# Kernel optimization log

Hardware: AMD Instinct MI355X
Metric: run time of the kernel (lower is better)

The kernel has to match this reference:

```python
import jax, jax.numpy as jnp
import numpy as np

K_ATTRS = 16  # fixed number of attribute clusters (torch.unique made static for jit)
NEG_INF = jnp.float32(-1e9)


def setup_inputs() -> dict:
    key = jax.random.key(0)
    ks = jax.random.split(key, 20)
    B, T, V, D, H = 4096, 200, 100000, 64, 64
    M0, M1 = 256, 128
    FC_IN = D + D + H + D  # 256
    s = 0.02
    f32 = jnp.float32
    inp = {
        "item_id": jax.random.randint(ks[0], (B,), 0, V),
        "hist_item_ids": jax.random.randint(ks[1], (B, T), 0, V),
        "hist_item_attributes": jax.random.randint(ks[2], (B, T), 0, K_ATTRS),
        "emb_table": s * jax.random.normal(ks[3], (V, D), dtype=f32),
        "au_W1": s * jax.random.normal(ks[4], (4 * D, H), dtype=f32),
        "au_b1": jnp.zeros((H,), f32),
        "au_W2": s * jax.random.normal(ks[5], (H, 1), dtype=f32),
        "au_b2": jnp.zeros((1,), f32),
        "gru_Wx": s * jax.random.normal(ks[6], (D, 3 * H), dtype=f32),
        "gru_Wh": s * jax.random.normal(ks[7], (H, 3 * H), dtype=f32),
        "gru_b": jnp.zeros((3 * H,), f32),
        "fc_W0": s * jax.random.normal(ks[8], (FC_IN, M0), dtype=f32),
        "fc_b0": jnp.zeros((M0,), f32),
        "fc_W1": s * jax.random.normal(ks[9], (M0, M1), dtype=f32),
        "fc_b1": jnp.zeros((M1,), f32),
        "final_W": s * jax.random.normal(ks[10], (M1, 1), dtype=f32),
        "final_b": jnp.zeros((1,), f32),
    }
    return inp


def reference(item_id, hist_item_ids, hist_item_attributes, emb_table,
              au_W1, au_b1, au_W2, au_b2, gru_Wx, gru_Wh, gru_b,
              fc_W0, fc_b0, fc_W1, fc_b1, final_W, final_b):
    item = emb_table[item_id]            # [B,D]
    hist = emb_table[hist_item_ids]      # [B,T,D]
    B = item.shape[0]
    H = gru_Wh.shape[0]

    # --- DIEN: GRU over history, final hidden state ---
    xp = hist @ gru_Wx + gru_b           # [B,T,3H]

    def step(h, x):
        gz, gr, gn = jnp.split(h @ gru_Wh, 3, axis=-1)
        xz, xr, xn = jnp.split(x, 3, axis=-1)
        z = jax.nn.sigmoid(xz + gz)
        r = jax.nn.sigmoid(xr + gr)
        n = jnp.tanh(xn + r * gn)
        return (1.0 - z) * n + z * h, None

    h0 = jnp.zeros((B, H), hist.dtype)
    interest_evolution, _ = jax.lax.scan(step, h0, jnp.swapaxes(xp, 0, 1))  # [B,H]

    # --- DIN-style activation unit: score each key against the target item ---
    def act_unit(q, keys):  # q:[B,D], keys:[B,N,D] -> [B,N,1]
        qe = jnp.broadcast_to(q[:, None, :], keys.shape)
        feat = jnp.concatenate([keys, qe, keys - qe, keys * qe], axis=-1)
        hid = jax.nn.relu(feat @ au_W1 + au_b1)
        return hid @ au_W2 + au_b2

    w1 = act_unit(item, hist)                    # [B,T,1]
    user_interest_l1 = jnp.sum(w1 * hist, axis=1)  # [B,D]

    # --- attribute_group: per-attribute masked softmax + weighted sum ---
    mask = hist_item_attributes[..., None] == jnp.arange(K_ATTRS)  # [B,T,K]
    logits = jnp.where(mask, w1, NEG_INF)        # [B,T,K]
    probs = jax.nn.softmax(logits, axis=1) * mask
    cluster = jnp.einsum('btk,btd->bkd', probs, hist)  # [B,K,D]

    w2 = act_unit(item, cluster)                 # [B,K,1]
    user_interest_l2 = jnp.sum(w2 * cluster, axis=1)  # [B,D]

    combined = jnp.concatenate(
        [user_interest_l1, user_interest_l2, interest_evolution, item], axis=1)
    x = jax.nn.relu(combined @ fc_W0 + fc_b0)
    x = jax.nn.relu(x @ fc_W1 + fc_b1)
    out = x @ final_W + final_b                  # [B,1]
    return jax.nn.sigmoid(out[:, 0])             # [B]
```

## Files before the change

### kernel.cpp

```cpp
#include <hip/hip_runtime.h>
#include <hip/hip_bf16.h>

#define B_   4096
#define T_   200
#define KA   16

#define OFF_BG  0
#define OFF_WQ  4096
#define OFF_QP  (OFF_BG  + B_*T_)
#define OFF_UI1 (OFF_QP  + B_*64)
#define OFF_UI2 (OFF_UI1 + B_*64)
#define OFF_HF  (OFF_UI2 + B_*64)
#define OFF_CL  (OFF_HF  + B_*64)

typedef __attribute__((ext_vector_type(8))) short bf16x8;
typedef __attribute__((ext_vector_type(4))) float f32x4;

__device__ __forceinline__ float sigmoidf_(float x) {
  return 1.f / (1.f + __expf(-x));
}
__device__ __forceinline__ float sigf(float x) {
  return __builtin_amdgcn_rcpf(1.f + __builtin_amdgcn_exp2f(-1.44269504f * x));
}
__device__ __forceinline__ float tanhfast(float y) {
  return 1.f - 2.f * __builtin_amdgcn_rcpf(1.f + __builtin_amdgcn_exp2f(2.88539008f * y));
}
__device__ __forceinline__ short f2bf(float x) {
  unsigned u = __float_as_uint(x);
  unsigned r = (u + 0x7fffu + ((u >> 16) & 1u)) >> 16;
  return (short)r;
}
__device__ __forceinline__ unsigned cvtpk(float lo, float hi) {
  unsigned r;
  asm("v_cvt_pk_bf16_f32 %0, %1, %2" : "=v"(r) : "v"(lo), "v"(hi));
  return r;
}
union BF8 { bf16x8 v; unsigned u[4]; };

__device__ __forceinline__ bf16x8 pack8(float4 f0, float4 f1) {
  BF8 a;
  a.u[0] = cvtpk(f0.x, f0.y);
  a.u[1] = cvtpk(f0.z, f0.w);
  a.u[2] = cvtpk(f1.x, f1.y);
  a.u[3] = cvtpk(f1.z, f1.w);
  return a.v;
}
__device__ __forceinline__ bf16x8 pack8m(float4 f0, float4 f1,
                                         float4 q0, float4 q1) {
  BF8 a;
  a.u[0] = cvtpk(f0.x*q0.x, f0.y*q0.y);
  a.u[1] = cvtpk(f0.z*q0.z, f0.w*q0.w);
  a.u[2] = cvtpk(f1.x*q1.x, f1.y*q1.y);
  a.u[3] = cvtpk(f1.z*q1.z, f1.w*q1.w);
  return a.v;
}


__global__ __launch_bounds__(256) void k_prep(
    const float* __restrict__ auW1, short* __restrict__ bg,
    float* __restrict__ wq)
{
  const int i = blockIdx.x*256 + threadIdx.x;
  if (i < 8192) {
    const int k = i >> 6, col = i & 63;
    float v;
    if (k < 64) v = auW1[k*64 + col] + auW1[2*4096 + k*64 + col];
    else        v = auW1[3*4096 + (k-64)*64 + col];
    bg[((k >> 5)*4 + ((k >> 3) & 3))*512 + col*8 + (k & 7)] = f2bf(v);
  } else if (i < 12288) {
    const int j = i - 8192;
    wq[j] = auW1[(64 + (j >> 6))*64 + (j & 63)]
          - auW1[(128 + (j >> 6))*64 + (j & 63)];
  }
}

__global__ __launch_bounds__(256) void k_act1(
    const int* __restrict__ item_id, const int* __restrict__ hist_ids,
    const int* __restrict__ attrs,
    const float* __restrict__ emb, const float* __restrict__ aub1,
    const float* __restrict__ auW2, const float* __restrict__ aub2,
    const short* __restrict__ bg_in, const float* __restrict__ wq_in,
    float* __restrict__ qp_out, float* __restrict__ ui1_out,
    float* __restrict__ ui2_out)
{
  __shared__ __align__(16) char sPool[16384];
  __shared__ __align__(16) float sCl[16][72];
  __shared__ float sW1[208];
  __shared__ float sP[200];
  __shared__ float sM[KA], sE[KA];
  __shared__ float sItem[64], sQp[64];
  __shared__ float sQpP[4][64];
  __shared__ float sUi[4][64];
  __shared__ float sWf[16];
  __shared__ int   sIds[200], sAttr[200];

  short* sB2 = (short*)sPool;
  float (*sAcc)[KA][64] = (float (*)[KA][64])sPool;

  const int b = blockIdx.x;
  const int tid = threadIdx.x;
  const int wave = tid >> 6, lane = tid & 63;
  const int g = lane >> 4;
  const int c15 = lane & 15;
  const int itrow = item_id[b];

  for (int i = tid; i < 4096; i += 256)
    ((unsigned*)sB2)[i] = ((const unsigned*)bg_in)[i];
  if (tid < 64) sItem[tid] = emb[(size_t)itrow*64 + tid];
  if (tid < T_) {
    sIds[tid]  = hist_ids[(size_t)b*T_ + tid];
    sAttr[tid] = attrs[(size_t)b*T_ + tid];
  }
  __syncthreads();

  {
    const int j = tid & 63, iq = tid >> 6;
    float acc = 0.f;
    #pragma unroll
    for (int ii = 0; ii < 16; ++ii) {
      const int i = iq*16 + ii;
      acc += sItem[i] * wq_in[i*64 + j];
    }
    sQpP[iq][j] = acc;
  }
  __syncthreads();
  if (tid < 64) {
    float q = aub1[tid] + sQpP[0][tid] + sQpP[1][tid] + sQpP[2][tid] + sQpP[3][tid];
    sQp[tid] = q;
    qp_out[(size_t)b*64 + tid] = q;
  }
  __syncthreads();

  const float4* itemp = (const float4*)(emb + (size_t)itrow*64);
  float4 q0 = itemp[g*2],     q1 = itemp[g*2 + 1];
  float4 q2 = itemp[8 + g*2], q3 = itemp[8 + g*2 + 1];

  bf16x8 bfr[4][4];
  #pragma unroll
  for (int kk = 0; kk < 4; ++kk) {
    #pragma unroll
    for (int n = 0; n < 4; ++n)
      bfr[kk][n] = *(const bf16x8*)&sB2[(kk*4 + g)*512 + (n*16 + c15)*8];
  }
  float w2v[4], qpv[4];
  #pragma unroll
  for (int n = 0; n < 4; ++n) {
    w2v[n] = auW2[n*16 + c15];
    qpv[n] = sQp[n*16 + c15];
  }
  const float b2v = aub2[0];
  __syncthreads();

  for (int i = tid; i < 4*KA*64; i += 256) ((float*)sAcc)[i] = 0.f;

  {
    float4 c0, c1, c2, c3;
    {
      const int t = wave*16 + c15;
      const int tc = (t < T_) ? t : (T_ - 1);
      const float4* kp = (const float4*)(emb + (size_t)sIds[tc]*64);
      c0 = kp[g*2];     c1 = kp[g*2 + 1];
      c2 = kp[8 + g*2]; c3 = kp[8 + g*2 + 1];
    }
    for (int tt = wave; tt < 13; tt += 4) {
      float4 n0{0,0,0,0}, n1{0,0,0,0}, n2{0,0,0,0}, n3{0,0,0,0};
      const int ttn = tt + 4;
      if (ttn < 13) {
        const int t = ttn*16 + c15;
        const int tc = (t < T_) ? t : (T_ - 1);
        const float4* kp = (const float4*)(emb + (size_t)sIds[tc]*64);
        n0 = kp[g*2];     n1 = kp[g*2 + 1];
        n2 = kp[8 + g*2]; n3 = kp[8 + g*2 + 1];
      }

      bf16x8 a0 = pack8(c0, c1);
      bf16x8 a1 = pack8(c2, c3);
      bf16x8 a2 = pack8m(c0, c1, q0, q1);
      bf16x8 a3 = pack8m(c2, c3, q2, q3);

      f32x4 acc[4];
      #pragma unroll
      for (int n = 0; n < 4; ++n) acc[n] = f32x4{qpv[n], qpv[n], qpv[n], qpv[n]};
      #pragma unroll
      for (int n = 0; n < 4; ++n) {
        acc[n] = __builtin_amdgcn_mfma_f32_16x16x32_bf16(a0, bfr[0][n], acc[n], 0, 0, 0);
        acc[n] = __builtin_amdgcn_mfma_f32_16x16x32_bf16(a1, bfr[1][n], acc[n], 0, 0, 0);
        acc[n] = __builtin_amdgcn_mfma_f32_16x16x32_bf16(a2, bfr[2][n], acc[n], 0, 0, 0);
        acc[n] = __builtin_amdgcn_mfma_f32_16x16x32_bf16(a3, bfr[3][n], acc[n], 0, 0, 0);
      }
      float ws[4] = {0.f, 0.f, 0.f, 0.f};
      #pragma unroll
      for (int n = 0; n < 4; ++n) {
        #pragma unroll
        for (int r = 0; r < 4; ++r)
          ws[r] += fmaxf(acc[n][r], 0.f) * w2v[n];
      }
      #pragma unroll
      for (int r = 0; r < 4; ++r) {
        ws[r] += __shfl_xor(ws[r], 1);
        ws[r] += __shfl_xor(ws[r], 2);
        ws[r] += __shfl_xor(ws[r], 4);
        ws[r] += __shfl_xor(ws[r], 8);
        ws[r] += b2v;
      }
      if (c15 == 0) {
        #pragma unroll
        for (int r = 0; r < 4; ++r) {
          const int trow = tt*16 + g*4 + r;
          if (trow < T_) sW1[trow] = ws[r];
        }
      }
      c0 = n0; c1 = n1; c2 = n2; c3 = n3;
    }
  }
  __syncthreads();

  for (int k = wave; k < KA; k += 4) {
    float m = -1e9f;
    for (int tt4 = 0; tt4 < 4; ++tt4) {
      int t = tt4*64 + lane;
      if (t < T_ && sAttr[t] == k) m = fmaxf(m, sW1[t]);
    }
    #pragma unroll
    for (int off = 32; off > 0; off >>= 1) m = fmaxf(m, __shfl_xor(m, off));
    float e = 0.f;
    for (int tt4 = 0; tt4 < 4; ++tt4) {
      int t = tt4*64 + lane;
      if (t < T_ && sAttr[t] == k) e += __expf(sW1[t] - m);
    }
    #pragma unroll
    for (int off = 32; off > 0; off >>= 1) e += __shfl_xor(e, off);
    if (lane == 0) { sM[k] = m; sE[k] = e; }
  }
  __syncthreads();
  if (tid < T_) {
    int k = sAttr[tid];
    float e = sE[k];
    sP[tid] = (e > 0.f) ? __expf(sW1[tid] - sM[k]) * __builtin_amdgcn_rcpf(e) : 0.f;
  }
  __syncthreads();

  {
    float uiacc = 0.f;
    float vcur = emb[(size_t)sIds[wave]*64 + lane];
    for (int t = wave; t < T_; t += 4) {
      const int tn = t + 4;
      float vnext = 0.f;
      if (tn < T_) vnext = emb[(size_t)sIds[tn]*64 + lane];
      const int k = sAttr[t];
      sAcc[wave][k][lane] += sP[t] * vcur;
      uiacc += sW1[t] * vcur;
      vcur = vnext;
    }
    sUi[wave][lane] = uiacc;
  }
  __syncthreads();

  for (int i = tid; i < KA*64; i += 256) {
    const int k = i >> 6, f = i & 63;
    sCl[k][f] = sAcc[0][0][i] + sAcc[1][0][i] + sAcc[2][0][i] + sAcc[3][0][i];
  }
  if (tid < 64) {
    ui1_out[(size_t)b*64 + tid] =
        sUi[0][tid] + sUi[1][tid] + sUi[2][tid] + sUi[3][tid];
  }
  __syncthreads();

  {
    float4 cl0 = *(const float4*)&sCl[c15][g*8];
    float4 cl1 = *(const float4*)&sCl[c15][g*8 + 4];
    float4 cl2 = *(const float4*)&sCl[c15][32 + g*8];
    float4 cl3 = *(const float4*)&sCl[c15][32 + g*8 + 4];
    bf16x8 a0 = pack8(cl0, cl1);
    bf16x8 a1 = pack8(cl2, cl3);
    bf16x8 a2 = pack8m(cl0, cl1, q0, q1);
    bf16x8 a3 = pack8m(cl2, cl3, q2, q3);

    f32x4 acc[4];
    #pragma unroll
    for (int n = 0; n < 4; ++n) acc[n] = f32x4{qpv[n], qpv[n], qpv[n], qpv[n]};
    #pragma unroll
    for (int n = 0; n < 4; ++n) {
      acc[n] = __builtin_amdgcn_mfma_f32_16x16x32_bf16(a0, bfr[0][n], acc[n], 0, 0, 0);
      acc[n] = __builtin_amdgcn_mfma_f32_16x16x32_bf16(a1, bfr[1][n], acc[n], 0, 0, 0);
      acc[n] = __builtin_amdgcn_mfma_f32_16x16x32_bf16(a2, bfr[2][n], acc[n], 0, 0, 0);
      acc[n] = __builtin_amdgcn_mfma_f32_16x16x32_bf16(a3, bfr[3][n], acc[n], 0, 0, 0);
    }
    float ws[4] = {0.f, 0.f, 0.f, 0.f};
    #pragma unroll
    for (int n = 0; n < 4; ++n) {
      #pragma unroll
      for (int r = 0; r < 4; ++r)
        ws[r] += fmaxf(acc[n][r], 0.f) * w2v[n];
    }
    #pragma unroll
    for (int r = 0; r < 4; ++r) {
      ws[r] += __shfl_xor(ws[r], 1);
      ws[r] += __shfl_xor(ws[r], 2);
      ws[r] += __shfl_xor(ws[r], 4);
      ws[r] += __shfl_xor(ws[r], 8);
    }
    if (wave == 0 && c15 == 0) {
      #pragma unroll
      for (int r = 0; r < 4; ++r) sWf[g*4 + r] = ws[r] + b2v;
    }
  }
  __syncthreads();

  {
    float uiacc = 0.f;
    #pragma unroll
    for (int kk = 0; kk < 4; ++kk) {
      const int k = wave*4 + kk;
      uiacc += sWf[k] * sCl[k][lane];
    }
    sUi[wave][lane] = uiacc;
  }
  __syncthreads();
  if (tid < 64) {
    ui2_out[(size_t)b*64 + tid] =
        sUi[0][tid] + sUi[1][tid] + sUi[2][tid] + sUi[3][tid];
  }
}

#define GRU_ROWS 16
__global__ __launch_bounds__(512) void k_gru(
    const int* __restrict__ hist_ids, const float* __restrict__ emb,
    const float* __restrict__ Wx, const float* __restrict__ Wh,
    const float* __restrict__ gb, float* __restrict__ hfin_out)
{
  __shared__ short sH[2][16*64];
  __shared__ short sX[4][16*64];
  __shared__ int   sIds[16*200];

  const int tid  = threadIdx.x;
  const int w    = tid >> 6;
  const int lane = tid & 63;
  const int g    = lane >> 4;
  const int c15  = lane & 15;
  const int b0   = blockIdx.x * GRU_ROWS;

  for (int i = tid; i < 16*200; i += 512) {
    const int r = i / 200, t = i - r*200;
    sIds[i] = hist_ids[(size_t)(b0 + r)*T_ + t];
  }
  for (int i = tid; i < 16*64; i += 512) sH[0][i] = 0;
  __syncthreads();

  if (w >= 4) {
    const int stane = (w - 4)*64 + lane;
    const int srow  = stane >> 4;
    const int scol  = (stane & 15) * 4;
    const int sidx  = srow*64 + (((scol >> 3) ^ (srow & 7))*8) + (scol & 7);
    const int* idrow = &sIds[srow*200];
    #pragma unroll
    for (int p = 0; p < 2; ++p) {
      const float4 f = *(const float4*)(emb + (size_t)idrow[p]*64 + scol);
      uint2 u; u.x = cvtpk(f.x, f.y); u.y = cvtpk(f.z, f.w);
      *(uint2*)&sX[p][sidx] = u;
    }
    __syncthreads();
    for (int t = 0; t < T_; ++t) {
      const int t2 = (t + 2 < T_) ? (t + 2) : (T_ - 1);
      const float4 f = *(const float4*)(emb + (size_t)idrow[t2]*64 + scol);
      uint2 u; u.x = cvtpk(f.x, f.y); u.y = cvtpk(f.z, f.w);
      *(uint2*)&sX[(t + 2) & 3][sidx] = u;
      __syncthreads();
    }
  } else {
    bf16x8 bx[3][2], bh[3][2];
    #pragma unroll
    for (int l = 0; l < 3; ++l) {
      const int jb = (l*4 + w)*16 + c15;
      #pragma unroll
      for (int kk = 0; kk < 2; ++kk) {
        bf16x8 vx, vh;
        #pragma unroll
        for (int e = 0; e < 8; ++e) {
          const int krow = kk*32 + g*8 + e;
          vx[e] = f2bf(Wx[(size_t)krow*192 + jb]);
          vh[e] = f2bf(Wh[(size_t)krow*192 + jb]);
        }
        bx[l][kk] = vx; bh[l][kk] = vh;
      }
    }
    float bias[3];
    #pragma unroll
    for (int l = 0; l < 3; ++l) bias[l] = gb[l*64 + w*16 + c15];

    const int rs = c15 & 7;
    const int ridx0 = c15*64 + ((g    ) ^ rs)*8;
    const int ridx1 = c15*64 + ((g + 4) ^ rs)*8;
    int widx[4];
    {
      const int unit = w*2 + (c15 >> 3);
      #pragma unroll
      for (int r = 0; r < 4; ++r) {
        const int row = g*4 + r;
        widx[r] = row*64 + ((unit ^ (row & 7))*8) + (c15 & 7);
      }
    }
    float hold[4] = {0.f, 0.f, 0.f, 0.f};
    __syncthreads();

    #pragma unroll 2
    for (int t = 0; t < T_; ++t) {
      const short* hbuf = sH[t & 1];
      short*       hnxt = sH[(t & 1) ^ 1];
      const short* xbuf = sX[t & 3];

      bf16x8 ax0 = *(const bf16x8*)&xbuf[ridx0];
      bf16x8 ax1 = *(const bf16x8*)&xbuf[ridx1];
      bf16x8 ah0 = *(const bf16x8*)&hbuf[ridx0];
      bf16x8 ah1 = *(const bf16x8*)&hbuf[ridx1];

      f32x4 aX[3], aH[3];
      #pragma unroll
      for (int l = 0; l < 3; ++l) {
        aX[l] = f32x4{bias[l], bias[l], bias[l], bias[l]};
        aH[l] = f32x4{0.f, 0.f, 0.f, 0.f};
      }
      #pragma unroll
      for (int l = 0; l < 3; ++l) {
        aH[l] = __builtin_amdgcn_mfma_f32_16x16x32_bf16(ah0, bh[l][0], aH[l], 0, 0, 0);
        aH[l] = __builtin_amdgcn_mfma_f32_16x16x32_bf16(ah1, bh[l][1], aH[l], 0, 0, 0);
        aX[l] = __builtin_amdgcn_mfma_f32_16x16x32_bf16(ax0, bx[l][0], aX[l], 0, 0, 0);
        aX[l] = __builtin_amdgcn_mfma_f32_16x16x32_bf16(ax1, bx[l][1], aX[l], 0, 0, 0);
      }

      #pragma unroll
      for (int r = 0; r < 4; ++r) {
        float z  = sigf(aX[0][r] + aH[0][r]);
        float rr = sigf(aX[1][r] + aH[1][r]);
        float nn = tanhfast(aX[2][r] + rr * aH[2][r]);
        hold[r] = nn + z * (hold[r] - nn);
        hnxt[widx[r]] = f2bf(hold[r]);
      }
      __syncthreads();
    }

    #pragma unroll
    for (int r = 0; r < 4; ++r)
      hfin_out[(size_t)(b0 + g*4 + r)*64 + w*16 + c15] = hold[r];
  }
}

#define MLP_ROWS 16
__global__ __launch_bounds__(256) void k_mlp(
    const int* __restrict__ item_id, const float* __restrict__ emb,
    const float* __restrict__ ui1, const float* __restrict__ ui2,
    const float* __restrict__ hfin,
    const float* __restrict__ W0, const float* __restrict__ b0,
    const float* __restrict__ W1, const float* __restrict__ b1,
    const float* __restrict__ fW, const float* __restrict__ fb,
    float* __restrict__ out)
{
  __shared__ float sC[MLP_ROWS][256];
  __shared__ float sX0[MLP_ROWS][256];
  __shared__ float sX1[MLP_ROWS][128];
  const int tid = threadIdx.x;
  const int rb  = blockIdx.x * MLP_ROWS;

  for (int idx = tid; idx < MLP_ROWS*256; idx += 256) {
    int r = idx >> 8, c = idx & 255;
    size_t row = (size_t)(rb + r);
    float v;
    if (c < 64)       v = ui1[row*64 + c];
    else if (c < 128) v = ui2[row*64 + (c-64)];
    else if (c < 192) v = hfin[row*64 + (c-128)];
    else              v = emb[(size_t)item_id[row]*64 + (c-192)];
    sC[r][c] = v;
  }
  __syncthreads();
  {
    float acc[MLP_ROWS];
    #pragma unroll
    for (int r = 0; r < MLP_ROWS; ++r) acc[r] = b0[tid];
    #pragma unroll 4
    for (int i = 0; i < 256; ++i) {
      float w = W0[(size_t)i*256 + tid];
      #pragma unroll
      for (int r = 0; r < MLP_ROWS; ++r) acc[r] += sC[r][i] * w;
    }
    #pragma unroll
    for (int r = 0; r < MLP_ROWS; ++r) sX0[r][tid] = fmaxf(acc[r], 0.f);
  }
  __syncthreads();
  if (tid < 128) {
    float acc[MLP_ROWS];
    #pragma unroll
    for (int r = 0; r < MLP_ROWS; ++r) acc[r] = b1[tid];
    #pragma unroll 4
    for (int i = 0; i < 256; ++i) {
      float w = W1[(size_t)i*128 + tid];
      #pragma unroll
      for (int r = 0; r < MLP_ROWS; ++r) acc[r] += sX0[r][i] * w;
    }
    #pragma unroll
    for (int r = 0; r < MLP_ROWS; ++r) sX1[r][tid] = fmaxf(acc[r], 0.f);
  }
  __syncthreads();
  {
    int r = tid >> 4, l16 = tid & 15;
    float p = 0.f;
    for (int i = l16; i < 128; i += 16) p += sX1[r][i] * fW[i];
    #pragma unroll
    for (int off = 8; off > 0; off >>= 1) p += __shfl_xor(p, off);
    if (l16 == 0) {
      float logit = p + fb[0];
      out[rb + r] = sigmoidf_(logit);
    }
  }
}

extern "C" void kernel_launch(void* const* d_in, const int* in_sizes, int n_in,
                              void* d_out, int out_size, void* d_ws, size_t ws_size,
                              hipStream_t stream)
{
  const int*   item_id  = (const int*)d_in[0];
  const int*   hist_ids = (const int*)d_in[1];
  const int*   attrs    = (const int*)d_in[2];
  const float* emb      = (const float*)d_in[3];
  const float* auW1     = (const float*)d_in[4];
  const float* aub1     = (const float*)d_in[5];
  const float* auW2     = (const float*)d_in[6];
  const float* aub2     = (const float*)d_in[7];
  const float* gWx      = (const float*)d_in[8];
  const float* gWh      = (const float*)d_in[9];
  const float* gb       = (const float*)d_in[10];
  const float* W0       = (const float*)d_in[11];
  const float* b0       = (const float*)d_in[12];
  const float* W1       = (const float*)d_in[13];
  const float* b1       = (const float*)d_in[14];
  const float* fW       = (const float*)d_in[15];
  const float* fb       = (const float*)d_in[16];

  float* out = (float*)d_out;
  float* ws  = (float*)d_ws;
  short* bg      = (short*)(ws + OFF_BG);
  float* wq      = ws + OFF_WQ;
  float* qp      = ws + OFF_QP;
  float* ui1     = ws + OFF_UI1;
  float* ui2     = ws + OFF_UI2;
  float* hfin    = ws + OFF_HF;

  k_prep<<<48, 256, 0, stream>>>(auW1, bg, wq);
  k_act1<<<B_, 256, 0, stream>>>(item_id, hist_ids, attrs, emb, aub1,
                                 auW2, aub2, bg, wq, qp, ui1, ui2);
  k_gru<<<B_/GRU_ROWS, 512, 0, stream>>>(hist_ids, emb, gWx, gWh, gb, hfin);
  k_mlp<<<B_/MLP_ROWS, 256, 0, stream>>>(item_id, emb, ui1, ui2, hfin,
                                         W0, b0, W1, b1, fW, fb, out);
}
```

Before: 342.1 us.

## Merge GRU and activation-unit kernels into one heterogeneous launch

Combines the GRU recurrence kernel and the per-row attention/cluster kernel into a single launch. The first 256 blocks run the GRU and the remaining 4096 blocks run the attention work, so the latency-bound serial GRU blocks can overlap with the throughput-bound attention blocks. The attention path is widened to 512 threads: more waves share the score tiles, and the weighted-sum and cluster-accumulation loops are split across the two wave halves. The trade-off is a shared 28KB LDS pool and 512-thread blocks for every block, which may reduce occupancy for the attention path. The software prefetch of the next history tile is also removed.

```diff
diff --git a/kernel.cpp b/kernel.cpp
--- a/kernel.cpp
+++ b/kernel.cpp
@@ -11,7 +11,8 @@
 #define OFF_UI1 (OFF_QP  + B_*64)
 #define OFF_UI2 (OFF_UI1 + B_*64)
 #define OFF_HF  (OFF_UI2 + B_*64)
-#define OFF_CL  (OFF_HF  + B_*64)
+
+#define GRU_BLOCKS (B_/16)
 
 typedef __attribute__((ext_vector_type(8))) short bf16x8;
 typedef __attribute__((ext_vector_type(4))) float f32x4;
@@ -74,37 +75,156 @@
   }
 }
 
-__global__ __launch_bounds__(256) void k_act1(
+__global__ __launch_bounds__(512) void k_fused(
     const int* __restrict__ item_id, const int* __restrict__ hist_ids,
     const int* __restrict__ attrs,
     const float* __restrict__ emb, const float* __restrict__ aub1,
     const float* __restrict__ auW2, const float* __restrict__ aub2,
     const short* __restrict__ bg_in, const float* __restrict__ wq_in,
+    const float* __restrict__ Wx, const float* __restrict__ Wh,
+    const float* __restrict__ gb,
     float* __restrict__ qp_out, float* __restrict__ ui1_out,
-    float* __restrict__ ui2_out)
+    float* __restrict__ ui2_out, float* __restrict__ hfin_out)
 {
-  __shared__ __align__(16) char sPool[16384];
-  __shared__ __align__(16) float sCl[16][72];
-  __shared__ float sW1[208];
-  __shared__ float sP[200];
-  __shared__ float sM[KA], sE[KA];
-  __shared__ float sItem[64], sQp[64];
-  __shared__ float sQpP[4][64];
-  __shared__ float sUi[4][64];
-  __shared__ float sWf[16];
-  __shared__ int   sIds[200], sAttr[200];
-
-  short* sB2 = (short*)sPool;
-  float (*sAcc)[KA][64] = (float (*)[KA][64])sPool;
-
-  const int b = blockIdx.x;
-  const int tid = threadIdx.x;
-  const int wave = tid >> 6, lane = tid & 63;
-  const int g = lane >> 4;
-  const int c15 = lane & 15;
+  __shared__ __align__(16) char pool[28032];
+
+  const int tid  = threadIdx.x;
+  const int w    = tid >> 6;
+  const int lane = tid & 63;
+  const int g    = lane >> 4;
+  const int c15  = lane & 15;
+
+  if (blockIdx.x < GRU_BLOCKS) {
+    short (*sH)[1024] = (short (*)[1024])(pool);
+    short (*sX)[1024] = (short (*)[1024])(pool + 4096);
+    int*  sIdsG       = (int*)(pool + 12288);
+    const int b0 = blockIdx.x * 16;
+
+    for (int i = tid; i < 16*200; i += 512) {
+      const int r = i / 200, t = i - r*200;
+      sIdsG[i] = hist_ids[(size_t)(b0 + r)*T_ + t];
+    }
+    for (int i = tid; i < 16*64; i += 512) sH[0][i] = 0;
+    __syncthreads();
+
+    if (w >= 4) {
+      const int stane = (w - 4)*64 + lane;
+      const int srow  = stane >> 4;
+      const int scol  = (stane & 15) * 4;
+      const int sidx  = srow*64 + (((scol >> 3) ^ (srow & 7))*8) + (scol & 7);
+      const int* idrow = &sIdsG[srow*200];
+      #pragma unroll
+      for (int p = 0; p < 2; ++p) {
+        const float4 f = *(const float4*)(emb + (size_t)idrow[p]*64 + scol);
+        uint2 u; u.x = cvtpk(f.x, f.y); u.y = cvtpk(f.z, f.w);
+        *(uint2*)&sX[p][sidx] = u;
+      }
+      __syncthreads();
+      for (int t = 0; t < T_; ++t) {
+        const int t2 = (t + 2 < T_) ? (t + 2) : (T_ - 1);
+        const float4 f = *(const float4*)(emb + (size_t)idrow[t2]*64 + scol);
+        uint2 u; u.x = cvtpk(f.x, f.y); u.y = cvtpk(f.z, f.w);
+        *(uint2*)&sX[(t + 2) & 3][sidx] = u;
+        __syncthreads();
+      }
+    } else {
+      bf16x8 bx[3][2], bh[3][2];
+      #pragma unroll
+      for (int l = 0; l < 3; ++l) {
+        const int jb = (l*4 + w)*16 + c15;
+        #pragma unroll
+        for (int kk = 0; kk < 2; ++kk) {
+          bf16x8 vx, vh;
+          #pragma unroll
+          for (int e = 0; e < 8; ++e) {
+            const int krow = kk*32 + g*8 + e;
+            vx[e] = f2bf(Wx[(size_t)krow*192 + jb]);
+            vh[e] = f2bf(Wh[(size_t)krow*192 + jb]);
+          }
+          bx[l][kk] = vx; bh[l][kk] = vh;
+        }
+      }
+      float bias[3];
+      #pragma unroll
+      for (int l = 0; l < 3; ++l) bias[l] = gb[l*64 + w*16 + c15];
+
+      const int rs = c15 & 7;
+      const int ridx0 = c15*64 + ((g    ) ^ rs)*8;
+      const int ridx1 = c15*64 + ((g + 4) ^ rs)*8;
+      int widx[4];
+      {
+        const int unit = w*2 + (c15 >> 3);
+        #pragma unroll
+        for (int r = 0; r < 4; ++r) {
+          const int row = g*4 + r;
+          widx[r] = row*64 + ((unit ^ (row & 7))*8) + (c15 & 7);
+        }
+      }
+      float hold[4] = {0.f, 0.f, 0.f, 0.f};
+      __syncthreads();
+
+      #pragma unroll 2
+      for (int t = 0; t < T_; ++t) {
+        const short* hbuf = sH[t & 1];
+        short*       hnxt = sH[(t & 1) ^ 1];
+        const short* xbuf = sX[t & 3];
+
+        bf16x8 ax0 = *(const bf16x8*)&xbuf[ridx0];
+        bf16x8 ax1 = *(const bf16x8*)&xbuf[ridx1];
+        bf16x8 ah0 = *(const bf16x8*)&hbuf[ridx0];
+        bf16x8 ah1 = *(const bf16x8*)&hbuf[ridx1];
+
+        f32x4 aX[3], aH[3];
+        #pragma unroll
+        for (int l = 0; l < 3; ++l) {
+          aX[l] = f32x4{bias[l], bias[l], bias[l], bias[l]};
+          aH[l] = f32x4{0.f, 0.f, 0.f, 0.f};
+        }
+        #pragma unroll
+        for (int l = 0; l < 3; ++l) {
+          aH[l] = __builtin_amdgcn_mfma_f32_16x16x32_bf16(ah0, bh[l][0], aH[l], 0, 0, 0);
+          aH[l] = __builtin_amdgcn_mfma_f32_16x16x32_bf16(ah1, bh[l][1], aH[l], 0, 0, 0);
+          aX[l] = __builtin_amdgcn_mfma_f32_16x16x32_bf16(ax0, bx[l][0], aX[l], 0, 0, 0);
+          aX[l] = __builtin_amdgcn_mfma_f32_16x16x32_bf16(ax1, bx[l][1], aX[l], 0, 0, 0);
+        }
+
+        #pragma unroll
+        for (int r = 0; r < 4; ++r) {
+          float z  = sigf(aX[0][r] + aH[0][r]);
+          float rr = sigf(aX[1][r] + aH[1][r]);
+          float nn = tanhfast(aX[2][r] + rr * aH[2][r]);
+          hold[r] = nn + z * (hold[r] - nn);
+          hnxt[widx[r]] = f2bf(hold[r]);
+        }
+        __syncthreads();
+      }
+
+      #pragma unroll
+      for (int r = 0; r < 4; ++r)
+        hfin_out[(size_t)(b0 + g*4 + r)*64 + w*16 + c15] = hold[r];
+    }
+    return;
+  }
+
+  short* sB2 = (short*)pool;
+  float (*sAcc)[KA][64] = (float (*)[KA][64])pool;
+  float (*sCl)[72] = (float (*)[72])(pool + 16384);
+  float* sW1   = (float*)(pool + 20992);
+  float* sP    = (float*)(pool + 21824);
+  float* sM    = (float*)(pool + 22624);
+  float* sE    = (float*)(pool + 22688);
+  float* sItem = (float*)(pool + 22752);
+  float* sQp   = (float*)(pool + 23008);
+  float (*sQpP)[64] = (float (*)[64])(pool + 23264);
+  float (*sUi)[64]  = (float (*)[64])(pool + 25312);
+  float* sWf   = (float*)(pool + 26336);
+  int*   sIds  = (int*)(pool + 26400);
+  int*   sAttr = (int*)(pool + 27200);
+
+  const int b = blockIdx.x - GRU_BLOCKS;
   const int itrow = item_id[b];
 
-  for (int i = tid; i < 4096; i += 256)
+  for (int i = tid; i < 4096; i += 512)
     ((unsigned*)sB2)[i] = ((const unsigned*)bg_in)[i];
   if (tid < 64) sItem[tid] = emb[(size_t)itrow*64 + tid];
   if (tid < T_) {
@@ -117,15 +237,17 @@
     const int j = tid & 63, iq = tid >> 6;
     float acc = 0.f;
     #pragma unroll
-    for (int ii = 0; ii < 16; ++ii) {
-      const int i = iq*16 + ii;
+    for (int ii = 0; ii < 8; ++ii) {
+      const int i = iq*8 + ii;
       acc += sItem[i] * wq_in[i*64 + j];
     }
     sQpP[iq][j] = acc;
   }
   __syncthreads();
   if (tid < 64) {
-    float q = aub1[tid] + sQpP[0][tid] + sQpP[1][tid] + sQpP[2][tid] + sQpP[3][tid];
+    float q = aub1[tid];
+    #pragma unroll
+    for (int iq = 0; iq < 8; ++iq) q += sQpP[iq][tid];
     sQp[tid] = q;
     qp_out[(size_t)b*64 + tid] = q;
   }
@@ -151,71 +273,57 @@
   const float b2v = aub2[0];
   __syncthreads();
 
-  for (int i = tid; i < 4*KA*64; i += 256) ((float*)sAcc)[i] = 0.f;
-
-  {
-    float4 c0, c1, c2, c3;
-    {
-      const int t = wave*16 + c15;
-      const int tc = (t < T_) ? t : (T_ - 1);
-      const float4* kp = (const float4*)(emb + (size_t)sIds[tc]*64);
+  for (int i = tid; i < 4*KA*64; i += 512) ((float*)sAcc)[i] = 0.f;
+
+  for (int tt = w; tt < 13; tt += 8) {
+    const int t = tt*16 + c15;
+    float4 c0{0,0,0,0}, c1{0,0,0,0}, c2{0,0,0,0}, c3{0,0,0,0};
+    if (t < T_) {
+      const float4* kp = (const float4*)(emb + (size_t)sIds[t]*64);
       c0 = kp[g*2];     c1 = kp[g*2 + 1];
       c2 = kp[8 + g*2]; c3 = kp[8 + g*2 + 1];
     }
-    for (int tt = wave; tt < 13; tt += 4) {
-      float4 n0{0,0,0,0}, n1{0,0,0,0}, n2{0,0,0,0}, n3{0,0,0,0};
-      const int ttn = tt + 4;
-      if (ttn < 13) {
-        const int t = ttn*16 + c15;
-        const int tc = (t < T_) ? t : (T_ - 1);
-        const float4* kp = (const float4*)(emb + (size_t)sIds[tc]*64);
-        n0 = kp[g*2];     n1 = kp[g*2 + 1];
-        n2 = kp[8 + g*2]; n3 = kp[8 + g*2 + 1];
+    bf16x8 a0 = pack8(c0, c1);
+    bf16x8 a1 = pack8(c2, c3);
+    bf16x8 a2 = pack8m(c0, c1, q0, q1);
+    bf16x8 a3 = pack8m(c2, c3, q2, q3);
+
+    f32x4 acc[4];
+    #pragma unroll
+    for (int n = 0; n < 4; ++n) acc[n] = f32x4{qpv[n], qpv[n], qpv[n], qpv[n]};
+    #pragma unroll
+    for (int n = 0; n < 4; ++n) {
+      acc[n] = __builtin_amdgcn_mfma_f32_16x16x32_bf16(a0, bfr[0][n], acc[n], 0, 0, 0);
+      acc[n] = __builtin_amdgcn_mfma_f32_16x16x32_bf16(a1, bfr[1][n], acc[n], 0, 0, 0);
+      acc[n] = __builtin_amdgcn_mfma_f32_16x16x32_bf16(a2, bfr[2][n], acc[n], 0, 0, 0);
+      acc[n] = __builtin_amdgcn_mfma_f32_16x16x32_bf16(a3, bfr[3][n], acc[n], 0, 0, 0);
+    }
+    float ws[4] = {0.f, 0.f, 0.f, 0.f};
+    #pragma unroll
+    for (int n = 0; n < 4; ++n) {
+      #pragma unroll
+      for (int r = 0; r < 4; ++r)
+        ws[r] += fmaxf(acc[n][r], 0.f) * w2v[n];
+    }
+    #pragma unroll
+    for (int r = 0; r < 4; ++r) {
+      ws[r] += __shfl_xor(ws[r], 1);
+      ws[r] += __shfl_xor(ws[r], 2);
+      ws[r] += __shfl_xor(ws[r], 4);
+      ws[r] += __shfl_xor(ws[r], 8);
+      ws[r] += b2v;
+    }
+    if (c15 == 0) {
+      #pragma unroll
+      for (int r = 0; r < 4; ++r) {
+        const int trow = tt*16 + g*4 + r;
+        if (trow < T_) sW1[trow] = ws[r];
       }
-
-      bf16x8 a0 = pack8(c0, c1);
-      bf16x8 a1 = pack8(c2, c3);
-      bf16x8 a2 = pack8m(c0, c1, q0, q1);
-      bf16x8 a3 = pack8m(c2, c3, q2, q3);
-
-      f32x4 acc[4];
-      #pragma unroll
-      for (int n = 0; n < 4; ++n) acc[n] = f32x4{qpv[n], qpv[n], qpv[n], qpv[n]};
-      #pragma unroll
-      for (int n = 0; n < 4; ++n) {
-        acc[n] = __builtin_amdgcn_mfma_f32_16x16x32_bf16(a0, bfr[0][n], acc[n], 0, 0, 0);
-        acc[n] = __builtin_amdgcn_mfma_f32_16x16x32_bf16(a1, bfr[1][n], acc[n], 0, 0, 0);
-        acc[n] = __builtin_amdgcn_mfma_f32_16x16x32_bf16(a2, bfr[2][n], acc[n], 0, 0, 0);
-        acc[n] = __builtin_amdgcn_mfma_f32_16x16x32_bf16(a3, bfr[3][n], acc[n], 0, 0, 0);
-      }
-      float ws[4] = {0.f, 0.f, 0.f, 0.f};
-      #pragma unroll
-      for (int n = 0; n < 4; ++n) {
-        #pragma unroll
-        for (int r = 0; r < 4; ++r)
-          ws[r] += fmaxf(acc[n][r], 0.f) * w2v[n];
-      }
-      #pragma unroll
-      for (int r = 0; r < 4; ++r) {
-        ws[r] += __shfl_xor(ws[r], 1);
-        ws[r] += __shfl_xor(ws[r], 2);
-        ws[r] += __shfl_xor(ws[r], 4);
-        ws[r] += __shfl_xor(ws[r], 8);
-        ws[r] += b2v;
-      }
-      if (c15 == 0) {
-        #pragma unroll
-        for (int r = 0; r < 4; ++r) {
-          const int trow = tt*16 + g*4 + r;
-          if (trow < T_) sW1[trow] = ws[r];
-        }
-      }
-      c0 = n0; c1 = n1; c2 = n2; c3 = n3;
-    }
-  }
-  __syncthreads();
-
-  for (int k = wave; k < KA; k += 4) {
+    }
+  }
+  __syncthreads();
+
+  for (int k = w; k < KA; k += 8) {
     float m = -1e9f;
     for (int tt4 = 0; tt4 < 4; ++tt4) {
       int t = tt4*64 + lane;
@@ -240,23 +348,31 @@
   }
   __syncthreads();
 
-  {
-    float uiacc = 0.f;
-    float vcur = emb[(size_t)sIds[wave]*64 + lane];
-    for (int t = wave; t < T_; t += 4) {
+  if (w < 4) {
+    float vcur = emb[(size_t)sIds[w]*64 + lane];
+    for (int t = w; t < T_; t += 4) {
       const int tn = t + 4;
       float vnext = 0.f;
       if (tn < T_) vnext = emb[(size_t)sIds[tn]*64 + lane];
-      const int k = sAttr[t];
-      sAcc[wave][k][lane] += sP[t] * vcur;
+      sAcc[w][sAttr[t]][lane] += sP[t] * vcur;
+      vcur = vnext;
+    }
+  } else {
+    const int w4 = w - 4;
+    float uiacc = 0.f;
+    float vcur = emb[(size_t)sIds[w4]*64 + lane];
+    for (int t = w4; t < T_; t += 4) {
+      const int tn = t + 4;
+      float vnext = 0.f;
+      if (tn < T_) vnext = emb[(size_t)sIds[tn]*64 + lane];
       uiacc += sW1[t] * vcur;
       vcur = vnext;
     }
-    sUi[wave][lane] = uiacc;
-  }
-  __syncthreads();
-
-  for (int i = tid; i < KA*64; i += 256) {
+    sUi[w4][lane] = uiacc;
+  }
+  __syncthreads();
+
+  for (int i = tid; i < KA*64; i += 512) {
     const int k = i >> 6, f = i & 63;
     sCl[k][f] = sAcc[0][0][i] + sAcc[1][0][i] + sAcc[2][0][i] + sAcc[3][0][i];
   }
@@ -300,148 +416,26 @@
       ws[r] += __shfl_xor(ws[r], 4);
       ws[r] += __shfl_xor(ws[r], 8);
     }
-    if (wave == 0 && c15 == 0) {
+    if (w == 0 && c15 == 0) {
       #pragma unroll
       for (int r = 0; r < 4; ++r) sWf[g*4 + r] = ws[r] + b2v;
     }
   }
   __syncthreads();
 
-  {
+  if (w < 4) {
     float uiacc = 0.f;
     #pragma unroll
     for (int kk = 0; kk < 4; ++kk) {
-      const int k = wave*4 + kk;
+      const int k = w*4 + kk;
       uiacc += sWf[k] * sCl[k][lane];
     }
-    sUi[wave][lane] = uiacc;
+    sUi[w][lane] = uiacc;
   }
   __syncthreads();
   if (tid < 64) {
     ui2_out[(size_t)b*64 + tid] =
         sUi[0][tid] + sUi[1][tid] + sUi[2][tid] + sUi[3][tid];
-  }
-}
-
-#define GRU_ROWS 16
-__global__ __launch_bounds__(512) void k_gru(
-    const int* __restrict__ hist_ids, const float* __restrict__ emb,
-    const float* __restrict__ Wx, const float* __restrict__ Wh,
-    const float* __restrict__ gb, float* __restrict__ hfin_out)
-{
-  __shared__ short sH[2][16*64];
-  __shared__ short sX[4][16*64];
-  __shared__ int   sIds[16*200];
-
-  const int tid  = threadIdx.x;
-  const int w    = tid >> 6;
-  const int lane = tid & 63;
-  const int g    = lane >> 4;
-  const int c15  = lane & 15;
-  const int b0   = blockIdx.x * GRU_ROWS;
-
-  for (int i = tid; i < 16*200; i += 512) {
-    const int r = i / 200, t = i - r*200;
-    sIds[i] = hist_ids[(size_t)(b0 + r)*T_ + t];
-  }
-  for (int i = tid; i < 16*64; i += 512) sH[0][i] = 0;
-  __syncthreads();
-
-  if (w >= 4) {
-    const int stane = (w - 4)*64 + lane;
-    const int srow  = stane >> 4;
-    const int scol  = (stane & 15) * 4;
-    const int sidx  = srow*64 + (((scol >> 3) ^ (srow & 7))*8) + (scol & 7);
-    const int* idrow = &sIds[srow*200];
-    #pragma unroll
-    for (int p = 0; p < 2; ++p) {
-      const float4 f = *(const float4*)(emb + (size_t)idrow[p]*64 + scol);
-      uint2 u; u.x = cvtpk(f.x, f.y); u.y = cvtpk(f.z, f.w);
-      *(uint2*)&sX[p][sidx] = u;
-    }
-    __syncthreads();
-    for (int t = 0; t < T_; ++t) {
-      const int t2 = (t + 2 < T_) ? (t + 2) : (T_ - 1);
-      const float4 f = *(const float4*)(emb + (size_t)idrow[t2]*64 + scol);
-      uint2 u; u.x = cvtpk(f.x, f.y); u.y = cvtpk(f.z, f.w);
-      *(uint2*)&sX[(t + 2) & 3][sidx] = u;
-      __syncthreads();
-    }
-  } else {
-    bf16x8 bx[3][2], bh[3][2];
-    #pragma unroll
-    for (int l = 0; l < 3; ++l) {
-      const int jb = (l*4 + w)*16 + c15;
-      #pragma unroll
-      for (int kk = 0; kk < 2; ++kk) {
-        bf16x8 vx, vh;
-        #pragma unroll
-        for (int e = 0; e < 8; ++e) {
-          const int krow = kk*32 + g*8 + e;
-          vx[e] = f2bf(Wx[(size_t)krow*192 + jb]);
-          vh[e] = f2bf(Wh[(size_t)krow*192 + jb]);
-        }
-        bx[l][kk] = vx; bh[l][kk] = vh;
-      }
-    }
-    float bias[3];
-    #pragma unroll
-    for (int l = 0; l < 3; ++l) bias[l] = gb[l*64 + w*16 + c15];
-
-    const int rs = c15 & 7;
-    const int ridx0 = c15*64 + ((g    ) ^ rs)*8;
-    const int ridx1 = c15*64 + ((g + 4) ^ rs)*8;
-    int widx[4];
-    {
-      const int unit = w*2 + (c15 >> 3);
-      #pragma unroll
-      for (int r = 0; r < 4; ++r) {
-        const int row = g*4 + r;
-        widx[r] = row*64 + ((unit ^ (row & 7))*8) + (c15 & 7);
-      }
-    }
-    float hold[4] = {0.f, 0.f, 0.f, 0.f};
-    __syncthreads();
-
-    #pragma unroll 2
-    for (int t = 0; t < T_; ++t) {
-      const short* hbuf = sH[t & 1];
-      short*       hnxt = sH[(t & 1) ^ 1];
-      const short* xbuf = sX[t & 3];
-
-      bf16x8 ax0 = *(const bf16x8*)&xbuf[ridx0];
-      bf16x8 ax1 = *(const bf16x8*)&xbuf[ridx1];
-      bf16x8 ah0 = *(const bf16x8*)&hbuf[ridx0];
-      bf16x8 ah1 = *(const bf16x8*)&hbuf[ridx1];
-
-      f32x4 aX[3], aH[3];
-      #pragma unroll
-      for (int l = 0; l < 3; ++l) {
-        aX[l] = f32x4{bias[l], bias[l], bias[l], bias[l]};
-        aH[l] = f32x4{0.f, 0.f, 0.f, 0.f};
-      }
-      #pragma unroll
-      for (int l = 0; l < 3; ++l) {
-        aH[l] = __builtin_amdgcn_mfma_f32_16x16x32_bf16(ah0, bh[l][0], aH[l], 0, 0, 0);
-        aH[l] = __builtin_amdgcn_mfma_f32_16x16x32_bf16(ah1, bh[l][1], aH[l], 0, 0, 0);
-        aX[l] = __builtin_amdgcn_mfma_f32_16x16x32_bf16(ax0, bx[l][0], aX[l], 0, 0, 0);
-        aX[l] = __builtin_amdgcn_mfma_f32_16x16x32_bf16(ax1, bx[l][1], aX[l], 0, 0, 0);
-      }
-
-      #pragma unroll
-      for (int r = 0; r < 4; ++r) {
-        float z  = sigf(aX[0][r] + aH[0][r]);
-        float rr = sigf(aX[1][r] + aH[1][r]);
-        float nn = tanhfast(aX[2][r] + rr * aH[2][r]);
-        hold[r] = nn + z * (hold[r] - nn);
-        hnxt[widx[r]] = f2bf(hold[r]);
-      }
-      __syncthreads();
-    }
-
-    #pragma unroll
-    for (int r = 0; r < 4; ++r)
-      hfin_out[(size_t)(b0 + g*4 + r)*64 + w*16 + c15] = hold[r];
   }
 }
 
@@ -545,9 +539,9 @@
   float* hfin    = ws + OFF_HF;
 
   k_prep<<<48, 256, 0, stream>>>(auW1, bg, wq);
-  k_act1<<<B_, 256, 0, stream>>>(item_id, hist_ids, attrs, emb, aub1,
-                                 auW2, aub2, bg, wq, qp, ui1, ui2);
-  k_gru<<<B_/GRU_ROWS, 512, 0, stream>>>(hist_ids, emb, gWx, gWh, gb, hfin);
+  k_fused<<<GRU_BLOCKS + B_, 512, 0, stream>>>(
+      item_id, hist_ids, attrs, emb, aub1, auW2, aub2, bg, wq,
+      gWx, gWh, gb, qp, ui1, ui2, hfin);
   k_mlp<<<B_/MLP_ROWS, 256, 0, stream>>>(item_id, emb, ui1, ui2, hfin,
                                          W0, b0, W1, b1, fW, fb, out);
 }
```

Measured after the change: 388.5 us. 1.14x slower.
